# Kernel tuning notes

Measured on AMD Instinct MI355X. Metric: run time of the kernel, lower is better.

## Reference

```python
import jax, jax.numpy as jnp
import numpy as np

DILATION_RATE = 4
SEGMENT_SIZE = 512


def setup_inputs() -> dict:
    key = jax.random.key(0)
    x = jax.random.normal(key, (4, 8192, 1024), dtype=jnp.float32)
    return {"x": x}


def reference(x):
    """LongNet-style dilated attention.

    For each offset in range(dilation_rate): take the strided slice
    x[:, offset::r, :], split it into segments of length `segment_size`,
    run full softmax(q k^T / sqrt(d)) v attention inside each segment
    (q=k=v=the slice; attention dim is the full d_model, matching how the
    original feeds [B, n_seg, seg, d_model] to FlashAttention), scatter the
    result back to the strided positions, and average the dilation heads
    (softmax over uniform logits == 1/r weights).

    Since seq_len % (r * segment_size) == 0, the r strided slices tile the
    sequence exactly, so we vectorize over offsets with a single reshape:
    position p = i*r + offset  ->  xr[:, i, offset, :].
    """
    r, seg = DILATION_RATE, SEGMENT_SIZE
    B, S, D = x.shape
    n = S // r            # tokens per strided slice
    g = n // seg          # segments per slice
    scale = 1.0 / jnp.sqrt(jnp.asarray(D, dtype=x.dtype))

    xs = x.reshape(B, g, seg, r, D)  # [B, g, seg, r, D]; axis r = dilation offset
    # segment-local attention, independently per (batch, offset, segment)
    scores = jnp.einsum("bgqrd,bgkrd->brgqk", xs, xs) * scale  # [B, r, g, seg, seg]
    probs = jax.nn.softmax(scores, axis=-1)
    out = jnp.einsum("brgqk,bgkrd->bgqrd", probs, xs)          # [B, g, seg, r, D]
    # scatter back to strided positions (pure reshape, since slices tile S),
    # then weighted sum with uniform softmax weights == divide by r.
    return out.reshape(B, S, D) / r
```

## Files before the change

### kernel.cpp

```cpp
#include <hip/hip_runtime.h>
#include <stdint.h>

typedef __bf16 bf16x8  __attribute__((ext_vector_type(8)));
typedef float  f32x4   __attribute__((ext_vector_type(4)));

#define LOG2E    1.44269504088896340736f
#define SM_SCALE 0.03125f

typedef __attribute__((address_space(1))) const uint32_t gau32;
typedef __attribute__((address_space(3))) uint32_t       lau32;
#define GLD16(g, l) __builtin_amdgcn_global_load_lds((gau32*)(g), (lau32*)(l), 16, 0, 0)

__device__ __forceinline__ uint32_t f2bf(float f) {
  uint32_t u = __builtin_bit_cast(uint32_t, f);
  u += 0x7FFFu + ((u >> 16) & 1u);
  return u >> 16;
}
__device__ __forceinline__ uint32_t pk2(float a, float b) {
  return f2bf(a) | (f2bf(b) << 16);
}
__device__ __forceinline__ uint4 pack8(float4 a, float4 b) {
  uint4 r;
  r.x = pk2(a.x, a.y); r.y = pk2(a.z, a.w);
  r.z = pk2(b.x, b.y); r.w = pk2(b.z, b.w);
  return r;
}

__global__ __launch_bounds__(256)
void prep_comb(const float* __restrict__ x, uint16_t* __restrict__ vt,
               uint16_t* __restrict__ xf) {
  __shared__ char tl[64 * 144];
  const int t    = threadIdx.x;
  const int blk  = blockIdx.x;
  const int dc   = blk & 15;
  const int kb   = (blk >> 4) & 7;
  const int prob = blk >> 7;
  const int b  = prob >> 4, off = (prob >> 2) & 3, gs = prob & 3;

  const int key = t >> 2, dq = t & 3;
  const float* src = x + ((size_t)(b * 8192 + gs * 2048 + (kb * 64 + key) * 4 + off)) * 1024
                     + dc * 64 + dq * 16;
  float4 f0 = *(const float4*)(src);
  float4 f1 = *(const float4*)(src + 4);
  float4 f2 = *(const float4*)(src + 8);
  float4 f3 = *(const float4*)(src + 12);
  const int swz = (key & 7) << 4;
  *(uint4*)(tl + key * 144 + ((dq * 32) ^ swz))      = pack8(f0, f1);
  *(uint4*)(tl + key * 144 + ((dq * 32 + 16) ^ swz)) = pack8(f2, f3);
  __syncthreads();
  {
    const int d = t >> 2, kq = t & 3;
    uint32_t w[8];
#pragma unroll
    for (int i = 0; i < 8; ++i) {
      int k0 = kq * 16 + 2 * i, k1 = k0 + 1;
      uint32_t a  = *(const uint16_t*)(tl + k0 * 144 + ((2 * d) ^ ((k0 & 7) << 4)));
      uint32_t bb = *(const uint16_t*)(tl + k1 * 144 + ((2 * d) ^ ((k1 & 7) << 4)));
      w[i] = a | (bb << 16);
    }
    uint16_t* dst = vt + ((size_t)(prob * 1024 + dc * 64 + d)) * 512 + kb * 64 + kq * 16;
    *(uint4*)(dst)     = *(uint4*)&w[0];
    *(uint4*)(dst + 8) = *(uint4*)&w[4];
  }
  {
    const int row = t >> 2, p = t & 3;
    const int dcl = p >> 1;
    const int dq8b = (p & 1) * 2;
    const int swz2 = (row & 7) << 4;
    char* fbase = (char*)xf +
        (((size_t)(prob * 32 + kb * 4 + (row >> 4)) * 32) + (dc * 2 + dcl)) * 1024;
#pragma unroll
    for (int i = 0; i < 2; ++i) {
      const int dq8 = dq8b + i;
      uint4 w = *(const uint4*)(tl + row * 144 + ((dcl * 64 + dq8 * 16) ^ swz2));
      *(uint4*)(fbase + ((row & 15) + 16 * dq8) * 16) = w;
    }
  }
}

#define R4_0 131072
#define R4_1 135168
#define LDS4_BYTES 139264

#define QKT_BODY(dc, A0, A1)                                                   \
  {                                                                            \
    const char* qb = smem + ((dc) >> 4) * 65536 + ((dc) & 15) * 4096 + lane16; \
    bf16x8 b0 = *(const bf16x8*)(qb);                                          \
    bf16x8 b1 = *(const bf16x8*)(qb + 1024);                                   \
    bf16x8 b2 = *(const bf16x8*)(qb + 2048);                                   \
    bf16x8 b3 = *(const bf16x8*)(qb + 3072);                                   \
    S[0][0] = __builtin_amdgcn_mfma_f32_16x16x32_bf16(A0, b0, S[0][0], 0, 0, 0); \
    S[0][1] = __builtin_amdgcn_mfma_f32_16x16x32_bf16(A0, b1, S[0][1], 0, 0, 0); \
    S[0][2] = __builtin_amdgcn_mfma_f32_16x16x32_bf16(A0, b2, S[0][2], 0, 0, 0); \
    S[0][3] = __builtin_amdgcn_mfma_f32_16x16x32_bf16(A0, b3, S[0][3], 0, 0, 0); \
    S[1][0] = __builtin_amdgcn_mfma_f32_16x16x32_bf16(A1, b0, S[1][0], 0, 0, 0); \
    S[1][1] = __builtin_amdgcn_mfma_f32_16x16x32_bf16(A1, b1, S[1][1], 0, 0, 0); \
    S[1][2] = __builtin_amdgcn_mfma_f32_16x16x32_bf16(A1, b2, S[1][2], 0, 0, 0); \
    S[1][3] = __builtin_amdgcn_mfma_f32_16x16x32_bf16(A1, b3, S[1][3], 0, 0, 0); \
  }

#define LOADA(dc, A0, A1) do {                       \
    A0 = *(const bf16x8*)(xfA0 + (dc) * 1024);       \
    A1 = *(const bf16x8*)(xfA1 + (dc) * 1024); } while (0)

__global__ __launch_bounds__(1024, 4)
void dilattn4(const char* __restrict__ xf, const char* __restrict__ vt,
              float* __restrict__ out) {
  extern __shared__ char smem[];

  const int tid  = threadIdx.x;
  const int lane = tid & 63;
  const int wid  = tid >> 6;
  const int h    = lane >> 4;
  const int l15  = lane & 15;
  const int psw  = (l15 & 7) << 4;
  const int lane16 = lane * 16;

  const int blk  = blockIdx.x;
  const int prob = ((blk & 7) << 3) | (blk >> 6);
  const int q0   = ((blk >> 3) & 7) * 64;
  const int b    = prob >> 4;
  const int off  = (prob >> 2) & 3;
  const int gs   = prob & 3;

  const char* xfp = xf + (size_t)prob * 1048576;
  const int qtile0 = q0 >> 4;

#pragma unroll
  for (int half = 0; half < 2; ++half)
#pragma unroll
    for (int i = 0; i < 4; ++i) {
      const int c = wid * 4 + i;
      const int dcl = c >> 2, qt = c & 3;
      const char* src = xfp + ((size_t)(qtile0 + qt) * 32 + (half * 16 + dcl)) * 1024 + lane16;
      GLD16(src, smem + half * 65536 + dcl * 4096 + qt * 1024);
    }

  const char* xfA0 = xfp + (size_t)(2 * wid) * 32768 + lane16;
  const char* xfA1 = xfA0 + 32768;

  f32x4 S[2][4];
#pragma unroll
  for (int i = 0; i < 2; ++i)
#pragma unroll
    for (int j = 0; j < 4; ++j) S[i][j] = (f32x4){0.f, 0.f, 0.f, 0.f};

  bf16x8 aP0, aP1, aQ0, aQ1;
  LOADA(0, aP0, aP1);
  LOADA(1, aQ0, aQ1);
  __syncthreads();

#pragma unroll
  for (int dc2 = 0; dc2 < 32; dc2 += 2) {
    QKT_BODY(dc2, aP0, aP1);
    if (dc2 + 2 < 32) LOADA(dc2 + 2, aP0, aP1);
    QKT_BODY(dc2 + 1, aQ0, aQ1);
    if (dc2 + 3 < 32) LOADA(dc2 + 3, aQ0, aQ1);
  }

  float mq[4], sq[4], rinv[4];
#pragma unroll
  for (int qt = 0; qt < 4; ++qt) {
    float m = S[0][qt][0];
#pragma unroll
    for (int kt = 0; kt < 2; ++kt)
#pragma unroll
      for (int r = 0; r < 4; ++r) m = fmaxf(m, S[kt][qt][r]);
    m = fmaxf(m, __shfl_xor(m, 16, 64));
    m = fmaxf(m, __shfl_xor(m, 32, 64));
    mq[qt] = m;
  }
  if (h == 0) {
#pragma unroll
    for (int qt = 0; qt < 4; ++qt)
      *(float*)(smem + R4_0 + (wid * 64 + 16 * qt + l15) * 4) = mq[qt];
  }
  __syncthreads();
#pragma unroll
  for (int qt = 0; qt < 4; ++qt) {
    float m = -3e38f;
#pragma unroll
    for (int w = 0; w < 16; ++w)
      m = fmaxf(m, *(const float*)(smem + R4_0 + (w * 64 + 16 * qt + l15) * 4));
    mq[qt] = m * SM_SCALE;
    sq[qt] = 0.f;
  }
#pragma unroll
  for (int kt = 0; kt < 2; ++kt)
#pragma unroll
    for (int qt = 0; qt < 4; ++qt)
#pragma unroll
      for (int r = 0; r < 4; ++r) {
        float v = exp2f((S[kt][qt][r] * SM_SCALE - mq[qt]) * LOG2E);
        S[kt][qt][r] = v;
        sq[qt] += v;
      }
#pragma unroll
  for (int qt = 0; qt < 4; ++qt) {
    sq[qt] += __shfl_xor(sq[qt], 16, 64);
    sq[qt] += __shfl_xor(sq[qt], 32, 64);
  }
  if (h == 0) {
#pragma unroll
    for (int qt = 0; qt < 4; ++qt)
      *(float*)(smem + R4_1 + (wid * 64 + 16 * qt + l15) * 4) = sq[qt];
  }
  __syncthreads();
#pragma unroll
  for (int qt = 0; qt < 4; ++qt) {
    float l = 0.f;
#pragma unroll
    for (int w = 0; w < 16; ++w)
      l += *(const float*)(smem + R4_1 + (w * 64 + 16 * qt + l15) * 4);
    rinv[qt] = 0.25f / l;
  }
#pragma unroll
  for (int kt = 0; kt < 2; ++kt)
#pragma unroll
    for (int qt = 0; qt < 4; ++qt) {
      uint2 w2;
      w2.x = pk2(S[kt][qt][0] * rinv[qt], S[kt][qt][1] * rinv[qt]);
      w2.y = pk2(S[kt][qt][2] * rinv[qt], S[kt][qt][3] * rinv[qt]);
      *(uint2*)(smem + (16 * qt + l15) * 1024 +
                ((64 * wid + 32 * kt + 8 * h) ^ psw)) = w2;
    }
  __syncthreads();

  f32x4 acc[4][4];
#pragma unroll
  for (int i = 0; i < 4; ++i)
#pragma unroll
    for (int j = 0; j < 4; ++j) acc[i][j] = (f32x4){0.f, 0.f, 0.f, 0.f};

  const char* vtW = vt + (size_t)prob * 1048576 + (size_t)(64 * wid + l15) * 1024 + 16 * h;
  const char* paB = smem + l15 * 1024;

#pragma unroll 2
  for (int ks = 0; ks < 16; ++ks) {
    bf16x8 v0 = *(const bf16x8*)(vtW + 0 * 16384 + ks * 64);
    bf16x8 v1 = *(const bf16x8*)(vtW + 1 * 16384 + ks * 64);
    bf16x8 v2 = *(const bf16x8*)(vtW + 2 * 16384 + ks * 64);
    bf16x8 v3 = *(const bf16x8*)(vtW + 3 * 16384 + ks * 64);
    bf16x8 pa[4];
#pragma unroll
    for (int qt = 0; qt < 4; ++qt)
      pa[qt] = *(const bf16x8*)(paB + qt * 16384 + ((64 * ks + 16 * h) ^ psw));
#pragma unroll
    for (int qt = 0; qt < 4; ++qt) {
      acc[0][qt] = __builtin_amdgcn_mfma_f32_16x16x32_bf16(pa[qt], v0, acc[0][qt], 0, 0, 0);
      acc[1][qt] = __builtin_amdgcn_mfma_f32_16x16x32_bf16(pa[qt], v1, acc[1][qt], 0, 0, 0);
      acc[2][qt] = __builtin_amdgcn_mfma_f32_16x16x32_bf16(pa[qt], v2, acc[2][qt], 0, 0, 0);
      acc[3][qt] = __builtin_amdgcn_mfma_f32_16x16x32_bf16(pa[qt], v3, acc[3][qt], 0, 0, 0);
    }
  }

  float* outW = out + ((size_t)(b * 8192 + gs * 2048 + (q0 + 4 * h) * 4 + off)) * 1024
                + 64 * wid + l15;
#pragma unroll
  for (int cd = 0; cd < 4; ++cd)
#pragma unroll
    for (int qt = 0; qt < 4; ++qt)
#pragma unroll
      for (int r = 0; r < 4; ++r)
        outW[(size_t)((16 * qt + r) * 4) * 1024 + cd * 16] = acc[cd][qt][r];
}

#define KP_OFF 0
#define Q_OFF  65536
#define RED0   65536
#define RED1   67584
#define LDS_BYTES 73728

__global__ __launch_bounds__(256)
void vt_prepass(const float* __restrict__ x, uint16_t* __restrict__ vt) {
  __shared__ char tl[64 * 144];
  const int t    = threadIdx.x;
  const int blk  = blockIdx.x;
  const int dc   = blk & 15;
  const int kb   = (blk >> 4) & 7;
  const int prob = blk >> 7;
  const int b  = prob >> 4, off = (prob >> 2) & 3, gs = prob & 3;

  const int key = t >> 2, dq = t & 3;
  const float* src = x + ((size_t)(b * 8192 + gs * 2048 + (kb * 64 + key) * 4 + off)) * 1024
                     + dc * 64 + dq * 16;
  float4 f0 = *(const float4*)(src);
  float4 f1 = *(const float4*)(src + 4);
  float4 f2 = *(const float4*)(src + 8);
  float4 f3 = *(const float4*)(src + 12);
  const int swz = (key & 7) << 4;
  *(uint4*)(tl + key * 144 + ((dq * 32) ^ swz))      = pack8(f0, f1);
  *(uint4*)(tl + key * 144 + ((dq * 32 + 16) ^ swz)) = pack8(f2, f3);
  __syncthreads();
  const int d = t >> 2, kq = t & 3;
  uint32_t w[8];
#pragma unroll
  for (int i = 0; i < 8; ++i) {
    int k0 = kq * 16 + 2 * i, k1 = k0 + 1;
    uint32_t a  = *(const uint16_t*)(tl + k0 * 144 + ((2 * d) ^ ((k0 & 7) << 4)));
    uint32_t bb = *(const uint16_t*)(tl + k1 * 144 + ((2 * d) ^ ((k1 & 7) << 4)));
    w[i] = a | (bb << 16);
  }
  uint16_t* dst = vt + ((size_t)(prob * 1024 + dc * 64 + d)) * 512 + kb * 64 + kq * 16;
  *(uint4*)(dst)     = *(uint4*)&w[0];
  *(uint4*)(dst + 8) = *(uint4*)&w[4];
}

template <int USE_VT>
__global__ __launch_bounds__(512, 2)
void dilattn2(const float* __restrict__ x, const uint16_t* __restrict__ vt,
              float* __restrict__ out) {
  extern __shared__ char smem[];

  const int tid  = threadIdx.x;
  const int lane = tid & 63;
  const int wid  = tid >> 6;
  const int h    = lane >> 4;
  const int l15  = lane & 15;
  const int psw  = (l15 & 7) << 4;

  const int blk  = blockIdx.x;
  const int prob = blk >> 3;
  const int q0   = (blk & 7) * 64;
  const int b    = prob >> 4;
  const int off  = (prob >> 2) & 3;
  const int gs   = prob & 3;

  const float* xb = x + (size_t)b * (8192u * 1024u);

  const int srow = tid >> 3;
  const int sg   = tid & 7;
  const float* gK = xb + (size_t)(gs * 2048 + srow * 4 + off) * 1024 + sg * 8;
  const float* gQ = xb + (size_t)(gs * 2048 + (q0 + srow) * 4 + off) * 1024 + sg * 8;
  const int kWr = srow * 128 + ((sg * 16) ^ ((srow & 7) << 4));
  const int qWr = Q_OFF + kWr;

  const int akR = (64 * wid + l15) * 128;
  const int bqR = Q_OFF + l15 * 128;
  const int fb0 = (16 * h) ^ psw;

  f32x4 S[4][4];
#pragma unroll
  for (int i = 0; i < 4; ++i)
#pragma unroll
    for (int j = 0; j < 4; ++j) S[i][j] = (f32x4){0.f, 0.f, 0.f, 0.f};

  float4 kp[16], qp[2];
#pragma unroll
  for (int j = 0; j < 8; ++j) {
    const float* p = gK + (size_t)j * 262144;
    kp[2 * j]     = *(const float4*)(p);
    kp[2 * j + 1] = *(const float4*)(p + 4);
  }
  qp[0] = *(const float4*)(gQ);
  qp[1] = *(const float4*)(gQ + 4);

#pragma unroll 1
  for (int dc = 0; dc < 16; ++dc) {
#pragma unroll
    for (int j = 0; j < 8; ++j)
      *(uint4*)(smem + KP_OFF + kWr + j * 8192) = pack8(kp[2 * j], kp[2 * j + 1]);
    *(uint4*)(smem + qWr) = pack8(qp[0], qp[1]);
    if (dc < 15) {
      const int doff = (dc + 1) * 64;
#pragma unroll
      for (int j = 0; j < 8; ++j) {
        const float* p = gK + (size_t)j * 262144 + doff;
        kp[2 * j]     = *(const float4*)(p);
        kp[2 * j + 1] = *(const float4*)(p + 4);
      }
      qp[0] = *(const float4*)(gQ + doff);
      qp[1] = *(const float4*)(gQ + doff + 4);
    }
    __syncthreads();
#pragma unroll
    for (int s = 0; s < 2; ++s) {
      const int fb = fb0 ^ (s << 6);
      bf16x8 aK[4], bq[4];
#pragma unroll
      for (int kt = 0; kt < 4; ++kt)
        aK[kt] = *(const bf16x8*)(smem + akR + kt * 2048 + fb);
#pragma unroll
      for (int qt = 0; qt < 4; ++qt)
        bq[qt] = *(const bf16x8*)(smem + bqR + qt * 2048 + fb);
#pragma unroll
      for (int kt = 0; kt < 4; ++kt)
#pragma unroll
        for (int qt = 0; qt < 4; ++qt)
          S[kt][qt] = __builtin_amdgcn_mfma_f32_16x16x32_bf16(aK[kt], bq[qt], S[kt][qt], 0, 0, 0);
    }
    __syncthreads();
  }

  float mq[4], sq[4], rinv[4];
#pragma unroll
  for (int qt = 0; qt < 4; ++qt) {
    float m = S[0][qt][0];
#pragma unroll
    for (int kt = 0; kt < 4; ++kt)
#pragma unroll
      for (int r = 0; r < 4; ++r) m = fmaxf(m, S[kt][qt][r]);
    m = fmaxf(m, __shfl_xor(m, 16, 64));
    m = fmaxf(m, __shfl_xor(m, 32, 64));
    mq[qt] = m;
  }
  if (h == 0) {
#pragma unroll
    for (int qt = 0; qt < 4; ++qt)
      *(float*)(smem + RED0 + (wid * 64 + 16 * qt + l15) * 4) = mq[qt];
  }
  __syncthreads();
#pragma unroll
  for (int qt = 0; qt < 4; ++qt) {
    float m = -3e38f;
#pragma unroll
    for (int w = 0; w < 8; ++w)
      m = fmaxf(m, *(const float*)(smem + RED0 + (w * 64 + 16 * qt + l15) * 4));
    mq[qt] = m * SM_SCALE;
    sq[qt] = 0.f;
  }
#pragma unroll
  for (int kt = 0; kt < 4; ++kt)
#pragma unroll
    for (int qt = 0; qt < 4; ++qt)
#pragma unroll
      for (int r = 0; r < 4; ++r) {
        float v = exp2f((S[kt][qt][r] * SM_SCALE - mq[qt]) * LOG2E);
        S[kt][qt][r] = v;
        sq[qt] += v;
      }
#pragma unroll
  for (int qt = 0; qt < 4; ++qt) {
    sq[qt] += __shfl_xor(sq[qt], 16, 64);
    sq[qt] += __shfl_xor(sq[qt], 32, 64);
  }
  if (h == 0) {
#pragma unroll
    for (int qt = 0; qt < 4; ++qt)
      *(float*)(smem + RED1 + (wid * 64 + 16 * qt + l15) * 4) = sq[qt];
  }
  __syncthreads();
#pragma unroll
  for (int qt = 0; qt < 4; ++qt) {
    float l = 0.f;
#pragma unroll
    for (int w = 0; w < 8; ++w)
      l += *(const float*)(smem + RED1 + (w * 64 + 16 * qt + l15) * 4);
    rinv[qt] = 0.25f / l;
  }
#pragma unroll
  for (int kt = 0; kt < 4; ++kt)
#pragma unroll
    for (int qt = 0; qt < 4; ++qt) {
      uint2 w2;
      w2.x = pk2(S[kt][qt][0] * rinv[qt], S[kt][qt][1] * rinv[qt]);
      w2.y = pk2(S[kt][qt][2] * rinv[qt], S[kt][qt][3] * rinv[qt]);
      *(uint2*)(smem + KP_OFF + (16 * qt + l15) * 1024 +
                ((128 * wid + 32 * kt + 8 * h) ^ psw)) = w2;
    }
  __syncthreads();

  f32x4 acc[8][4];
#pragma unroll
  for (int i = 0; i < 8; ++i)
#pragma unroll
    for (int j = 0; j < 4; ++j) acc[i][j] = (f32x4){0.f, 0.f, 0.f, 0.f};

  const uint16_t* vtW = nullptr;
  if constexpr (USE_VT)
    vtW = vt + ((size_t)(prob * 1024 + 128 * wid + l15)) * 512 + 8 * h;

#pragma unroll 1
  for (int ks = 0; ks < 16; ++ks) {
    bf16x8 pa[4];
#pragma unroll
    for (int qt = 0; qt < 4; ++qt)
      pa[qt] = *(const bf16x8*)(smem + KP_OFF + (16 * qt + l15) * 1024 +
                                ((64 * ks + 16 * h) ^ psw));
#pragma unroll
    for (int cd = 0; cd < 8; ++cd) {
      bf16x8 v;
      if constexpr (USE_VT) {
        v = *(const bf16x8*)(vtW + (size_t)((cd >> 2) * 64 + (cd & 3) * 16) * 512 + 32 * ks);
      } else {
        const int d = 128 * wid + (cd >> 2) * 64 + (cd & 3) * 16 + l15;
        union { bf16x8 v; uint16_t u[8]; } a0;
#pragma unroll
        for (int jj = 0; jj < 8; ++jj) {
          int key = 32 * ks + 8 * h + jj;
          a0.u[jj] = (uint16_t)f2bf(xb[(size_t)(gs * 2048 + key * 4 + off) * 1024 + d]);
        }
        v = a0.v;
      }
#pragma unroll
      for (int qt = 0; qt < 4; ++qt)
        acc[cd][qt] = __builtin_amdgcn_mfma_f32_16x16x32_bf16(pa[qt], v, acc[cd][qt], 0, 0, 0);
    }
  }

#pragma unroll
  for (int cd = 0; cd < 8; ++cd) {
    const int d = 128 * wid + (cd >> 2) * 64 + (cd & 3) * 16 + l15;
#pragma unroll
    for (int qt = 0; qt < 4; ++qt)
#pragma unroll
      for (int r = 0; r < 4; ++r) {
        const int qq = q0 + 16 * qt + 4 * h + r;
        out[((size_t)(b * 8192 + gs * 2048 + qq * 4 + off)) * 1024 + d] = acc[cd][qt][r];
      }
  }
}

extern "C" void kernel_launch(void* const* d_in, const int* in_sizes, int n_in,
                              void* d_out, int out_size, void* d_ws, size_t ws_size,
                              hipStream_t stream) {
  const float* x = (const float*)d_in[0];
  float* out = (float*)d_out;
  (void)in_sizes; (void)n_in; (void)out_size;
  const size_t vt_bytes = 64ull * 1024 * 512 * 2;
  const size_t xf_bytes = 64ull * 1024 * 1024;
  if (ws_size >= vt_bytes + xf_bytes) {
    uint16_t* vtp = (uint16_t*)d_ws;
    uint16_t* xfp = (uint16_t*)((char*)d_ws + vt_bytes);
    hipFuncSetAttribute(reinterpret_cast<const void*>(dilattn4),
                        hipFuncAttributeMaxDynamicSharedMemorySize, LDS4_BYTES);
    prep_comb<<<8192, 256, 0, stream>>>(x, vtp, xfp);
    dilattn4<<<512, 1024, LDS4_BYTES, stream>>>((const char*)xfp, (const char*)vtp, out);
  } else if (ws_size >= vt_bytes) {
    uint16_t* vtp = (uint16_t*)d_ws;
    hipFuncSetAttribute(reinterpret_cast<const void*>(dilattn2<1>),
                        hipFuncAttributeMaxDynamicSharedMemorySize, LDS_BYTES);
    vt_prepass<<<8192, 256, 0, stream>>>(x, vtp);
    dilattn2<1><<<512, 512, LDS_BYTES, stream>>>(x, vtp, out);
  } else {
    hipFuncSetAttribute(reinterpret_cast<const void*>(dilattn2<0>),
                        hipFuncAttributeMaxDynamicSharedMemorySize, LDS_BYTES);
    dilattn2<0><<<512, 512, LDS_BYTES, stream>>>(x, nullptr, out);
  }
}
```

Baseline: 185.0 us.

## Halve block to 512 threads, stage Q in two halves to cut LDS

The attention kernel now runs with 8 waves instead of 16. Each wave computes 4 key tiles in QK^T and 128 output columns in PV, done as two sequential 64-column passes. The Q tile is staged into LDS in two halves of the head dimension with a barrier in between, which drops the LDS footprint from about 136KB to about 68KB. This should allow more blocks per CU, or at least less LDS pressure, and fewer waves per reduction. In exchange there are extra syncs, more registers per wave, and only half as many waves to hide latency.

```diff
diff --git a/kernel.cpp b/kernel.cpp
--- a/kernel.cpp
+++ b/kernel.cpp
@@ -78,33 +78,41 @@
   }
 }
 
-#define R4_0 131072
-#define R4_1 135168
-#define LDS4_BYTES 139264
-
-#define QKT_BODY(dc, A0, A1)                                                   \
-  {                                                                            \
-    const char* qb = smem + ((dc) >> 4) * 65536 + ((dc) & 15) * 4096 + lane16; \
-    bf16x8 b0 = *(const bf16x8*)(qb);                                          \
-    bf16x8 b1 = *(const bf16x8*)(qb + 1024);                                   \
-    bf16x8 b2 = *(const bf16x8*)(qb + 2048);                                   \
-    bf16x8 b3 = *(const bf16x8*)(qb + 3072);                                   \
-    S[0][0] = __builtin_amdgcn_mfma_f32_16x16x32_bf16(A0, b0, S[0][0], 0, 0, 0); \
-    S[0][1] = __builtin_amdgcn_mfma_f32_16x16x32_bf16(A0, b1, S[0][1], 0, 0, 0); \
-    S[0][2] = __builtin_amdgcn_mfma_f32_16x16x32_bf16(A0, b2, S[0][2], 0, 0, 0); \
-    S[0][3] = __builtin_amdgcn_mfma_f32_16x16x32_bf16(A0, b3, S[0][3], 0, 0, 0); \
-    S[1][0] = __builtin_amdgcn_mfma_f32_16x16x32_bf16(A1, b0, S[1][0], 0, 0, 0); \
-    S[1][1] = __builtin_amdgcn_mfma_f32_16x16x32_bf16(A1, b1, S[1][1], 0, 0, 0); \
-    S[1][2] = __builtin_amdgcn_mfma_f32_16x16x32_bf16(A1, b2, S[1][2], 0, 0, 0); \
-    S[1][3] = __builtin_amdgcn_mfma_f32_16x16x32_bf16(A1, b3, S[1][3], 0, 0, 0); \
-  }
-
-#define LOADA(dc, A0, A1) do {                       \
-    A0 = *(const bf16x8*)(xfA0 + (dc) * 1024);       \
-    A1 = *(const bf16x8*)(xfA1 + (dc) * 1024); } while (0)
-
-__global__ __launch_bounds__(1024, 4)
-void dilattn4(const char* __restrict__ xf, const char* __restrict__ vt,
+#define R5_0 65536
+#define R5_1 67584
+#define LDS5_BYTES 69632
+
+#define QKT5(dc, A)                                                              \
+  {                                                                              \
+    const char* qb = smem + ((dc) & 15) * 4096 + lane16;                         \
+    bf16x8 b0 = *(const bf16x8*)(qb);                                            \
+    bf16x8 b1 = *(const bf16x8*)(qb + 1024);                                     \
+    bf16x8 b2 = *(const bf16x8*)(qb + 2048);                                     \
+    bf16x8 b3 = *(const bf16x8*)(qb + 3072);                                     \
+    _Pragma("unroll")                                                            \
+    for (int kt = 0; kt < 4; ++kt) {                                             \
+      S[kt][0] = __builtin_amdgcn_mfma_f32_16x16x32_bf16(A[kt], b0, S[kt][0], 0, 0, 0); \
+      S[kt][1] = __builtin_amdgcn_mfma_f32_16x16x32_bf16(A[kt], b1, S[kt][1], 0, 0, 0); \
+      S[kt][2] = __builtin_amdgcn_mfma_f32_16x16x32_bf16(A[kt], b2, S[kt][2], 0, 0, 0); \
+      S[kt][3] = __builtin_amdgcn_mfma_f32_16x16x32_bf16(A[kt], b3, S[kt][3], 0, 0, 0); \
+    }                                                                            \
+  }
+
+#define LOADA5(dc, A) do {                                                       \
+    _Pragma("unroll")                                                            \
+    for (int kt = 0; kt < 4; ++kt)                                               \
+      A[kt] = *(const bf16x8*)(xfA + kt * 32768 + (dc) * 1024); } while (0)
+
+#define STAGE_HALF(half) do {                                                    \
+    _Pragma("unroll")                                                            \
+    for (int i = 0; i < 8; ++i) {                                                \
+      const int c = wid * 8 + i;                                                 \
+      const int dcl = c >> 2, qt = c & 3;                                        \
+      GLD16(xfp + ((size_t)(qtile0 + qt) * 32 + ((half) * 16 + dcl)) * 1024 + lane16, \
+            smem + dcl * 4096 + qt * 1024); } } while (0)
+
+__global__ __launch_bounds__(512, 4)
+void dilattn5(const char* __restrict__ xf, const char* __restrict__ vt,
               float* __restrict__ out) {
   extern __shared__ char smem[];
 
@@ -125,37 +133,35 @@
 
   const char* xfp = xf + (size_t)prob * 1048576;
   const int qtile0 = q0 >> 4;
-
-#pragma unroll
-  for (int half = 0; half < 2; ++half)
-#pragma unroll
-    for (int i = 0; i < 4; ++i) {
-      const int c = wid * 4 + i;
-      const int dcl = c >> 2, qt = c & 3;
-      const char* src = xfp + ((size_t)(qtile0 + qt) * 32 + (half * 16 + dcl)) * 1024 + lane16;
-      GLD16(src, smem + half * 65536 + dcl * 4096 + qt * 1024);
-    }
-
-  const char* xfA0 = xfp + (size_t)(2 * wid) * 32768 + lane16;
-  const char* xfA1 = xfA0 + 32768;
-
-  f32x4 S[2][4];
-#pragma unroll
-  for (int i = 0; i < 2; ++i)
+  const char* xfA = xfp + (size_t)(4 * wid) * 32768 + lane16;
+
+  f32x4 S[4][4];
+#pragma unroll
+  for (int i = 0; i < 4; ++i)
 #pragma unroll
     for (int j = 0; j < 4; ++j) S[i][j] = (f32x4){0.f, 0.f, 0.f, 0.f};
 
-  bf16x8 aP0, aP1, aQ0, aQ1;
-  LOADA(0, aP0, aP1);
-  LOADA(1, aQ0, aQ1);
-  __syncthreads();
-
-#pragma unroll
-  for (int dc2 = 0; dc2 < 32; dc2 += 2) {
-    QKT_BODY(dc2, aP0, aP1);
-    if (dc2 + 2 < 32) LOADA(dc2 + 2, aP0, aP1);
-    QKT_BODY(dc2 + 1, aQ0, aQ1);
-    if (dc2 + 3 < 32) LOADA(dc2 + 3, aQ0, aQ1);
+  STAGE_HALF(0);
+  bf16x8 aP[4], aQ[4];
+  LOADA5(0, aP);
+  LOADA5(1, aQ);
+  __syncthreads();
+#pragma unroll
+  for (int dc2 = 0; dc2 < 16; dc2 += 2) {
+    QKT5(dc2, aP);
+    LOADA5(dc2 + 2, aP);
+    QKT5(dc2 + 1, aQ);
+    LOADA5(dc2 + 3, aQ);
+  }
+  __syncthreads();
+  STAGE_HALF(1);
+  __syncthreads();
+#pragma unroll
+  for (int dc2 = 16; dc2 < 32; dc2 += 2) {
+    QKT5(dc2, aP);
+    if (dc2 + 2 < 32) LOADA5(dc2 + 2, aP);
+    QKT5(dc2 + 1, aQ);
+    if (dc2 + 3 < 32) LOADA5(dc2 + 3, aQ);
   }
 
   float mq[4], sq[4], rinv[4];
@@ -163,7 +169,7 @@
   for (int qt = 0; qt < 4; ++qt) {
     float m = S[0][qt][0];
 #pragma unroll
-    for (int kt = 0; kt < 2; ++kt)
+    for (int kt = 0; kt < 4; ++kt)
 #pragma unroll
       for (int r = 0; r < 4; ++r) m = fmaxf(m, S[kt][qt][r]);
     m = fmaxf(m, __shfl_xor(m, 16, 64));
@@ -173,20 +179,20 @@
   if (h == 0) {
 #pragma unroll
     for (int qt = 0; qt < 4; ++qt)
-      *(float*)(smem + R4_0 + (wid * 64 + 16 * qt + l15) * 4) = mq[qt];
+      *(float*)(smem + R5_0 + (wid * 64 + 16 * qt + l15) * 4) = mq[qt];
   }
   __syncthreads();
 #pragma unroll
   for (int qt = 0; qt < 4; ++qt) {
     float m = -3e38f;
 #pragma unroll
-    for (int w = 0; w < 16; ++w)
-      m = fmaxf(m, *(const float*)(smem + R4_0 + (w * 64 + 16 * qt + l15) * 4));
+    for (int w = 0; w < 8; ++w)
+      m = fmaxf(m, *(const float*)(smem + R5_0 + (w * 64 + 16 * qt + l15) * 4));
     mq[qt] = m * SM_SCALE;
     sq[qt] = 0.f;
   }
 #pragma unroll
-  for (int kt = 0; kt < 2; ++kt)
+  for (int kt = 0; kt < 4; ++kt)
 #pragma unroll
     for (int qt = 0; qt < 4; ++qt)
 #pragma unroll
@@ -203,66 +209,68 @@
   if (h == 0) {
 #pragma unroll
     for (int qt = 0; qt < 4; ++qt)
-      *(float*)(smem + R4_1 + (wid * 64 + 16 * qt + l15) * 4) = sq[qt];
+      *(float*)(smem + R5_1 + (wid * 64 + 16 * qt + l15) * 4) = sq[qt];
   }
   __syncthreads();
 #pragma unroll
   for (int qt = 0; qt < 4; ++qt) {
     float l = 0.f;
 #pragma unroll
-    for (int w = 0; w < 16; ++w)
-      l += *(const float*)(smem + R4_1 + (w * 64 + 16 * qt + l15) * 4);
+    for (int w = 0; w < 8; ++w)
+      l += *(const float*)(smem + R5_1 + (w * 64 + 16 * qt + l15) * 4);
     rinv[qt] = 0.25f / l;
   }
 #pragma unroll
-  for (int kt = 0; kt < 2; ++kt)
+  for (int kt = 0; kt < 4; ++kt)
 #pragma unroll
     for (int qt = 0; qt < 4; ++qt) {
       uint2 w2;
       w2.x = pk2(S[kt][qt][0] * rinv[qt], S[kt][qt][1] * rinv[qt]);
       w2.y = pk2(S[kt][qt][2] * rinv[qt], S[kt][qt][3] * rinv[qt]);
       *(uint2*)(smem + (16 * qt + l15) * 1024 +
-                ((64 * wid + 32 * kt + 8 * h) ^ psw)) = w2;
-    }
-  __syncthreads();
-
-  f32x4 acc[4][4];
-#pragma unroll
-  for (int i = 0; i < 4; ++i)
-#pragma unroll
-    for (int j = 0; j < 4; ++j) acc[i][j] = (f32x4){0.f, 0.f, 0.f, 0.f};
-
-  const char* vtW = vt + (size_t)prob * 1048576 + (size_t)(64 * wid + l15) * 1024 + 16 * h;
+                ((128 * wid + 32 * kt + 8 * h) ^ psw)) = w2;
+    }
+  __syncthreads();
+
   const char* paB = smem + l15 * 1024;
-
+#pragma unroll 1
+  for (int p = 0; p < 2; ++p) {
+    const int dbase = 128 * wid + 64 * p;
+    f32x4 acc[4][4];
+#pragma unroll
+    for (int i = 0; i < 4; ++i)
+#pragma unroll
+      for (int j = 0; j < 4; ++j) acc[i][j] = (f32x4){0.f, 0.f, 0.f, 0.f};
+
+    const char* vtW = vt + (size_t)prob * 1048576 + (size_t)(dbase + l15) * 1024 + 16 * h;
 #pragma unroll 2
-  for (int ks = 0; ks < 16; ++ks) {
-    bf16x8 v0 = *(const bf16x8*)(vtW + 0 * 16384 + ks * 64);
-    bf16x8 v1 = *(const bf16x8*)(vtW + 1 * 16384 + ks * 64);
-    bf16x8 v2 = *(const bf16x8*)(vtW + 2 * 16384 + ks * 64);
-    bf16x8 v3 = *(const bf16x8*)(vtW + 3 * 16384 + ks * 64);
-    bf16x8 pa[4];
-#pragma unroll
-    for (int qt = 0; qt < 4; ++qt)
-      pa[qt] = *(const bf16x8*)(paB + qt * 16384 + ((64 * ks + 16 * h) ^ psw));
-#pragma unroll
-    for (int qt = 0; qt < 4; ++qt) {
-      acc[0][qt] = __builtin_amdgcn_mfma_f32_16x16x32_bf16(pa[qt], v0, acc[0][qt], 0, 0, 0);
-      acc[1][qt] = __builtin_amdgcn_mfma_f32_16x16x32_bf16(pa[qt], v1, acc[1][qt], 0, 0, 0);
-      acc[2][qt] = __builtin_amdgcn_mfma_f32_16x16x32_bf16(pa[qt], v2, acc[2][qt], 0, 0, 0);
-      acc[3][qt] = __builtin_amdgcn_mfma_f32_16x16x32_bf16(pa[qt], v3, acc[3][qt], 0, 0, 0);
-    }
-  }
-
-  float* outW = out + ((size_t)(b * 8192 + gs * 2048 + (q0 + 4 * h) * 4 + off)) * 1024
-                + 64 * wid + l15;
-#pragma unroll
-  for (int cd = 0; cd < 4; ++cd)
-#pragma unroll
-    for (int qt = 0; qt < 4; ++qt)
-#pragma unroll
-      for (int r = 0; r < 4; ++r)
-        outW[(size_t)((16 * qt + r) * 4) * 1024 + cd * 16] = acc[cd][qt][r];
+    for (int ks = 0; ks < 16; ++ks) {
+      bf16x8 v0 = *(const bf16x8*)(vtW + 0 * 16384 + ks * 64);
+      bf16x8 v1 = *(const bf16x8*)(vtW + 1 * 16384 + ks * 64);
+      bf16x8 v2 = *(const bf16x8*)(vtW + 2 * 16384 + ks * 64);
+      bf16x8 v3 = *(const bf16x8*)(vtW + 3 * 16384 + ks * 64);
+      bf16x8 pa[4];
+#pragma unroll
+      for (int qt = 0; qt < 4; ++qt)
+        pa[qt] = *(const bf16x8*)(paB + qt * 16384 + ((64 * ks + 16 * h) ^ psw));
+#pragma unroll
+      for (int qt = 0; qt < 4; ++qt) {
+        acc[0][qt] = __builtin_amdgcn_mfma_f32_16x16x32_bf16(pa[qt], v0, acc[0][qt], 0, 0, 0);
+        acc[1][qt] = __builtin_amdgcn_mfma_f32_16x16x32_bf16(pa[qt], v1, acc[1][qt], 0, 0, 0);
+        acc[2][qt] = __builtin_amdgcn_mfma_f32_16x16x32_bf16(pa[qt], v2, acc[2][qt], 0, 0, 0);
+        acc[3][qt] = __builtin_amdgcn_mfma_f32_16x16x32_bf16(pa[qt], v3, acc[3][qt], 0, 0, 0);
+      }
+    }
+    float* outW = out + ((size_t)(b * 8192 + gs * 2048 + (q0 + 4 * h) * 4 + off)) * 1024
+                  + dbase + l15;
+#pragma unroll
+    for (int cd = 0; cd < 4; ++cd)
+#pragma unroll
+      for (int qt = 0; qt < 4; ++qt)
+#pragma unroll
+        for (int r = 0; r < 4; ++r)
+          outW[(size_t)((16 * qt + r) * 4) * 1024 + cd * 16] = acc[cd][qt][r];
+  }
 }
 
 #define KP_OFF 0
@@ -522,10 +530,10 @@
   if (ws_size >= vt_bytes + xf_bytes) {
     uint16_t* vtp = (uint16_t*)d_ws;
     uint16_t* xfp = (uint16_t*)((char*)d_ws + vt_bytes);
-    hipFuncSetAttribute(reinterpret_cast<const void*>(dilattn4),
-                        hipFuncAttributeMaxDynamicSharedMemorySize, LDS4_BYTES);
+    hipFuncSetAttribute(reinterpret_cast<const void*>(dilattn5),
+                        hipFuncAttributeMaxDynamicSharedMemorySize, LDS5_BYTES);
     prep_comb<<<8192, 256, 0, stream>>>(x, vtp, xfp);
-    dilattn4<<<512, 1024, LDS4_BYTES, stream>>>((const char*)xfp, (const char*)vtp, out);
+    dilattn5<<<512, 512, LDS5_BYTES, stream>>>((const char*)xfp, (const char*)vtp, out);
   } else if (ws_size >= vt_bytes) {
     uint16_t* vtp = (uint16_t*)d_ws;
     hipFuncSetAttribute(reinterpret_cast<const void*>(dilattn2<1>),
```

New measurement: 189.5 us. 2.4% more time.
